# Performance work log

Measured on AMD Instinct MI355X. Metric: run time of the kernel, lower is better.

## Reference

```python
import jax, jax.numpy as jnp
import numpy as np

N_NODES = 50000
N_EDGES = 600000
DIN, DH, DOUT = 128, 256, 128
BN_EPS = 1e-5
LRELU_SLOPE = 0.01


def setup_inputs() -> dict:
    key = jax.random.key(0)
    ks = jax.random.split(key, 16)
    rn = lambda k, s, sc=0.05: jax.random.normal(k, s, dtype=jnp.float32) * sc
    return {
        'nodes': jax.random.normal(ks[0], (N_NODES, DIN), dtype=jnp.float32),
        'src': jax.random.randint(ks[1], (N_EDGES,), 0, N_NODES, dtype=jnp.int32),
        'dst': jax.random.randint(ks[2], (N_EDGES,), 0, N_NODES, dtype=jnp.int32),
        # FeedForward params
        'Wf1': rn(ks[3], (DIN, DH)), 'bf1': jnp.zeros((DH,), jnp.float32),
        'gf1': jnp.ones((DH,), jnp.float32), 'bef1': jnp.zeros((DH,), jnp.float32),
        'Wf2': rn(ks[4], (DH, DIN)), 'bf2': jnp.zeros((DIN,), jnp.float32),
        'gf2': jnp.ones((DIN,), jnp.float32), 'bef2': jnp.zeros((DIN,), jnp.float32),
        # SAGEConv 1 (in->hidden)
        'Ws1': rn(ks[5], (DIN, DH)), 'Wn1': rn(ks[6], (DIN, DH)), 'b1': jnp.zeros((DH,), jnp.float32),
        'gs1': jnp.ones((DH,), jnp.float32), 'bs1': jnp.zeros((DH,), jnp.float32),
        # SAGEConv 2 (hidden->out)
        'Ws2': rn(ks[7], (DH, DOUT)), 'Wn2': rn(ks[8], (DH, DOUT)), 'b2': jnp.zeros((DOUT,), jnp.float32),
        'gs2': jnp.ones((DOUT,), jnp.float32), 'bs2': jnp.zeros((DOUT,), jnp.float32),
    }


def _bn(x, gamma, beta):
    # BatchNorm1d, training mode: batch stats over node dim, biased variance
    mu = jnp.mean(x, axis=0)
    var = jnp.mean(jnp.square(x - mu), axis=0)
    return (x - mu) * jax.lax.rsqrt(var + BN_EPS) * gamma + beta


def _sage_mean(x, src, dst, Wself, Wneigh, bias):
    # DGL SAGEConv('mean'): out = x@Wself + mean_{src->dst}(x[src])@Wneigh + bias
    n = x.shape[0]
    deg = jax.ops.segment_sum(jnp.ones_like(src, dtype=x.dtype), dst, num_segments=n)
    agg = jax.ops.segment_sum(x[src], dst, num_segments=n)  # [N, d] irregular scatter-add
    h_neigh = agg / jnp.maximum(deg, 1.0)[:, None]
    return x @ Wself + h_neigh @ Wneigh + bias


def reference(nodes, src, dst, Wf1, bf1, gf1, bef1, Wf2, bf2, gf2, bef2,
              Ws1, Wn1, b1, gs1, bs1, Ws2, Wn2, b2, gs2, bs2):
    # FeedForward (dropout=0 -> identity)
    h = jax.nn.relu(_bn(nodes @ Wf1 + bf1, gf1, bef1))
    h = jax.nn.relu(_bn(h @ Wf2 + bf2, gf2, bef2))
    # SAGE layer 1
    h1 = _sage_mean(h, src, dst, Ws1, Wn1, b1)
    h1 = jax.nn.leaky_relu(_bn(h1, gs1, bs1), LRELU_SLOPE)
    # SAGE layer 2
    h2 = _sage_mean(h1, src, dst, Ws2, Wn2, b2)
    return jax.nn.leaky_relu(_bn(h2, gs2, bs2), LRELU_SLOPE)
```

## Files before the change

### kernel.cpp

```cpp
#include <hip/hip_runtime.h>

#define DIN 128
#define BN_EPS 1e-5f

typedef __attribute__((ext_vector_type(8))) short bf16x8;
typedef __attribute__((ext_vector_type(8))) unsigned short us8;
typedef __attribute__((ext_vector_type(4))) float f32x4;

__device__ __forceinline__ ushort f2bf(float f) {
    unsigned u = __float_as_uint(f);
    u += 0x7fffu + ((u >> 16) & 1u);
    return (ushort)(u >> 16);
}
__device__ __forceinline__ float bf2f(ushort h) {
    return __uint_as_float(((unsigned)h) << 16);
}

template<int KC, int NT, int STATS>
__global__ __launch_bounds__(256) void gemm_lds(
    const ushort* __restrict__ A, const ushort* __restrict__ BT,
    ushort* __restrict__ C, int mStrips, int N,
    float* __restrict__ gsums, float* __restrict__ gsqs)
{
    constexpr int K = KC * 32;
    constexpr int CPR = KC * 4;
    constexpr int LOGCPR = (KC == 4) ? 4 : 5;
    constexpr int LPL = KC / 4;
    __shared__ ushort abuf[16 * K];

    int tid = threadIdx.x;
    int lane = tid & 63;
    int w = tid >> 6;
    int cl = lane & 15, q = lane >> 4;
    int colBase = w * (16 * NT);
    int chBase = w * (16 * KC);

    bf16x8 bf[NT][KC];
    #pragma unroll
    for (int nt = 0; nt < NT; nt++) {
        const ushort* bp = BT + (long)(colBase + nt * 16 + cl) * K + q * 8;
        #pragma unroll
        for (int kc = 0; kc < KC; kc++)
            bf[nt][kc] = *(const bf16x8*)(bp + kc * 32);
    }

    float ssum[NT], ssq[NT];
    #pragma unroll
    for (int nt = 0; nt < NT; nt++) { ssum[nt] = 0.f; ssq[nt] = 0.f; }

    int totalSets = gridDim.x;
    int s0 = blockIdx.x;

    us8 stg[LPL];
    {
        const ushort* As = A + (long)s0 * 16 * K;
        #pragma unroll
        for (int u = 0; u < LPL; u++)
            stg[u] = *(const us8*)(As + (chBase + u * 64 + lane) * 8);
        #pragma unroll
        for (int u = 0; u < LPL; u++) {
            int ch = chBase + u * 64 + lane;
            int r = ch >> LOGCPR;
            int c = ch & (CPR - 1);
            *(us8*)(abuf + (((r << LOGCPR) + (c ^ (r & 7))) * 8)) = stg[u];
        }
    }
    __syncthreads();

    for (int s = s0; s < mStrips; s += totalSets) {
        int nxt = s + totalSets;
        bool more = nxt < mStrips;
        if (more) {
            const ushort* As = A + (long)nxt * 16 * K;
            #pragma unroll
            for (int u = 0; u < LPL; u++)
                stg[u] = *(const us8*)(As + (chBase + u * 64 + lane) * 8);
        }
        bf16x8 af[KC];
        #pragma unroll
        for (int kc = 0; kc < KC; kc++)
            af[kc] = *(const bf16x8*)(abuf + (((cl << LOGCPR) + ((kc * 4 + q) ^ (cl & 7))) * 8));
        f32x4 acc[NT] = {};
        #pragma unroll
        for (int kc = 0; kc < KC; kc++)
            #pragma unroll
            for (int nt = 0; nt < NT; nt++)
                acc[nt] = __builtin_amdgcn_mfma_f32_16x16x32_bf16(af[kc], bf[nt][kc], acc[nt], 0, 0, 0);
        int rowBase = s * 16;
        #pragma unroll
        for (int nt = 0; nt < NT; nt++) {
            #pragma unroll
            for (int r = 0; r < 4; r++) {
                float v = acc[nt][r];
                long row = rowBase + q * 4 + r;
                C[row * N + colBase + nt * 16 + cl] = f2bf(v);
                if (STATS) { ssum[nt] += v; ssq[nt] += v * v; }
            }
        }
        __syncthreads();
        if (more) {
            #pragma unroll
            for (int u = 0; u < LPL; u++) {
                int ch = chBase + u * 64 + lane;
                int r = ch >> LOGCPR;
                int c = ch & (CPR - 1);
                *(us8*)(abuf + (((r << LOGCPR) + (c ^ (r & 7))) * 8)) = stg[u];
            }
        }
        __syncthreads();
    }

    if (STATS) {
        #pragma unroll
        for (int nt = 0; nt < NT; nt++) {
            ssum[nt] += __shfl_xor(ssum[nt], 16, 64);
            ssum[nt] += __shfl_xor(ssum[nt], 32, 64);
            ssq[nt]  += __shfl_xor(ssq[nt], 16, 64);
            ssq[nt]  += __shfl_xor(ssq[nt], 32, 64);
        }
        if (q == 0) {
            #pragma unroll
            for (int nt = 0; nt < NT; nt++) {
                atomicAdd(&gsums[colBase + nt * 16 + cl], ssum[nt]);
                atomicAdd(&gsqs[colBase + nt * 16 + cl], ssq[nt]);
            }
        }
    }
}

__global__ __launch_bounds__(256) void setup_all(
    const float* __restrict__ nodes, ushort* __restrict__ Xbf, int nConv4, int nbConv,
    const float* __restrict__ W0, const float* __restrict__ W1,
    const float* __restrict__ W2, const float* __restrict__ W3,
    const float* __restrict__ W4, const float* __restrict__ W5,
    ushort* __restrict__ WT,
    int* __restrict__ zeroInts, int nZero4, int nbZero,
    float* __restrict__ stats)
{
    int b = blockIdx.x;
    int tid = threadIdx.x;
    if (b < nbConv) {
        int t = b * 256 + tid;
        if (t < nConv4) {
            float4 v = *(const float4*)&nodes[(long)t * 4];
            ushort4 o; o.x = f2bf(v.x); o.y = f2bf(v.y); o.z = f2bf(v.z); o.w = f2bf(v.w);
            *(ushort4*)&Xbf[(long)t * 4] = o;
        }
        return;
    }
    b -= nbConv;
    if (b < 768) {
        int seg = b >> 7;
        const float* W; int logK, dstBase, stride, kOff;
        switch (seg) {
            case 0: W = W0; logK = 7; dstBase = 0;      stride = 128; kOff = 0;   break;
            case 1: W = W1; logK = 8; dstBase = 32768;  stride = 256; kOff = 0;   break;
            case 2: W = W2; logK = 7; dstBase = 65536;  stride = 256; kOff = 0;   break;
            case 3: W = W3; logK = 7; dstBase = 65536;  stride = 256; kOff = 128; break;
            case 4: W = W4; logK = 8; dstBase = 131072; stride = 256; kOff = 0;   break;
            default:W = W5; logK = 8; dstBase = 163840; stride = 256; kOff = 0;   break;
        }
        int t = (b & 127) * 256 + tid;
        int N = 32768 >> logK;
        int k = t & ((1 << logK) - 1);
        int n = t >> logK;
        WT[(long)dstBase + (long)n * stride + kOff + k] = f2bf(W[(long)k * N + n]);
        return;
    }
    b -= 768;
    if (b < nbZero) {
        int t = b * 256 + tid;
        if (t < nZero4) *(int4*)&zeroInts[(long)t * 4] = make_int4(0, 0, 0, 0);
        return;
    }
    b -= nbZero;
    int t = b * 256 + tid;
    if (t < 512) *(float4*)&stats[(long)t * 4] = make_float4(0, 0, 0, 0);
}

template<int LOGN>
__global__ __launch_bounds__(256) void bnact_bf16(
    const ushort* __restrict__ X,
    const float* __restrict__ sums, const float* __restrict__ sqs,
    const float* __restrict__ gamma, const float* __restrict__ beta, float invM,
    ushort* __restrict__ O, int nRows, int outStride, float negSlope)
{
    constexpr int NCH = 1 << LOGN;
    __shared__ float ssc[NCH], ssh[NCH];
    int tid = threadIdx.x;
    if (tid < NCH) {
        float mean = sums[tid] * invM;
        float var = sqs[tid] * invM - mean * mean;
        float sc = gamma[tid] * rsqrtf(var + BN_EPS);
        ssc[tid] = sc;
        ssh[tid] = beta[tid] - mean * sc;
    }
    __syncthreads();
    int cb = (tid * 8) & (NCH - 1);
    float4 sA = *(const float4*)&ssc[cb];
    float4 sB = *(const float4*)&ssc[cb + 4];
    float4 hA = *(const float4*)&ssh[cb];
    float4 hB = *(const float4*)&ssh[cb + 4];
    const int rpb = (256 * 8) >> LOGN;
    int r0 = blockIdx.x * rpb + ((tid * 8) >> LOGN);
    int rstride = gridDim.x * rpb;
    for (int row = r0; row < nRows; row += rstride) {
        us8 v = *(const us8*)&X[(long)row * NCH + cb];
        float f0 = bf2f(v[0]) * sA.x + hA.x; f0 = (f0 > 0.f) ? f0 : f0 * negSlope;
        float f1 = bf2f(v[1]) * sA.y + hA.y; f1 = (f1 > 0.f) ? f1 : f1 * negSlope;
        float f2 = bf2f(v[2]) * sA.z + hA.z; f2 = (f2 > 0.f) ? f2 : f2 * negSlope;
        float f3 = bf2f(v[3]) * sA.w + hA.w; f3 = (f3 > 0.f) ? f3 : f3 * negSlope;
        float f4 = bf2f(v[4]) * sB.x + hB.x; f4 = (f4 > 0.f) ? f4 : f4 * negSlope;
        float f5 = bf2f(v[5]) * sB.y + hB.y; f5 = (f5 > 0.f) ? f5 : f5 * negSlope;
        float f6 = bf2f(v[6]) * sB.z + hB.z; f6 = (f6 > 0.f) ? f6 : f6 * negSlope;
        float f7 = bf2f(v[7]) * sB.w + hB.w; f7 = (f7 > 0.f) ? f7 : f7 * negSlope;
        us8 o;
        o[0] = f2bf(f0); o[1] = f2bf(f1); o[2] = f2bf(f2); o[3] = f2bf(f3);
        o[4] = f2bf(f4); o[5] = f2bf(f5); o[6] = f2bf(f6); o[7] = f2bf(f7);
        *(us8*)&O[(long)row * outStride + cb] = o;
    }
}

__global__ __launch_bounds__(256) void bnact_f32(
    float* __restrict__ X,
    const float* __restrict__ sums, const float* __restrict__ sqs,
    const float* __restrict__ gamma, const float* __restrict__ beta, float invM,
    int nRows, float negSlope)
{
    __shared__ float ssc[128], ssh[128];
    int tid = threadIdx.x;
    if (tid < 128) {
        float mean = sums[tid] * invM;
        float var = sqs[tid] * invM - mean * mean;
        float sc = gamma[tid] * rsqrtf(var + BN_EPS);
        ssc[tid] = sc;
        ssh[tid] = beta[tid] - mean * sc;
    }
    __syncthreads();
    int cb = (tid * 4) & 127;
    float4 sc = *(const float4*)&ssc[cb];
    float4 sh = *(const float4*)&ssh[cb];
    int r0 = blockIdx.x * 8 + ((tid * 4) >> 7);
    int rstride = gridDim.x * 8;
    for (int row = r0; row < nRows; row += rstride) {
        float4 v = *(const float4*)&X[(long)row * 128 + cb];
        float a = v.x * sc.x + sh.x; a = (a > 0.f) ? a : a * negSlope;
        float b = v.y * sc.y + sh.y; b = (b > 0.f) ? b : b * negSlope;
        float d = v.z * sc.z + sh.z; d = (d > 0.f) ? d : d * negSlope;
        float e = v.w * sc.w + sh.w; e = (e > 0.f) ? e : e * negSlope;
        *(float4*)&X[(long)row * 128 + cb] = make_float4(a, b, d, e);
    }
}

__global__ __launch_bounds__(256) void colstats128(
    const float* __restrict__ X, float* __restrict__ sums, float* __restrict__ sqs, int M)
{
    __shared__ float ss[128], sq[128];
    int tid = threadIdx.x;
    if (tid < 128) { ss[tid] = 0.f; sq[tid] = 0.f; }
    __syncthreads();
    int cg = tid & 31;
    int worker = (blockIdx.x << 3) | (tid >> 5);
    int totalW = gridDim.x << 3;
    float4 s4 = make_float4(0, 0, 0, 0), q4 = make_float4(0, 0, 0, 0);
    for (int r = worker; r < M; r += totalW) {
        float4 v = *(const float4*)&X[(long)r * 128 + cg * 4];
        s4.x += v.x; s4.y += v.y; s4.z += v.z; s4.w += v.w;
        q4.x += v.x * v.x; q4.y += v.y * v.y; q4.z += v.z * v.z; q4.w += v.w * v.w;
    }
    atomicAdd(&ss[cg * 4 + 0], s4.x); atomicAdd(&sq[cg * 4 + 0], q4.x);
    atomicAdd(&ss[cg * 4 + 1], s4.y); atomicAdd(&sq[cg * 4 + 1], q4.y);
    atomicAdd(&ss[cg * 4 + 2], s4.z); atomicAdd(&sq[cg * 4 + 2], q4.z);
    atomicAdd(&ss[cg * 4 + 3], s4.w); atomicAdd(&sq[cg * 4 + 3], q4.w);
    __syncthreads();
    if (tid < 128) { atomicAdd(&sums[tid], ss[tid]); atomicAdd(&sqs[tid], sq[tid]); }
}

__global__ void degcount_kernel(const int* __restrict__ dst, int* __restrict__ degi, int E)
{
    int i = blockIdx.x * blockDim.x + threadIdx.x;
    if (i < E) atomicAdd(&degi[dst[i]], 1);
}

__global__ __launch_bounds__(256) void scan_block_sums(const int* __restrict__ degi,
                                                       int* __restrict__ partial, int n)
{
    __shared__ int s[256];
    int i = blockIdx.x * 256 + threadIdx.x;
    s[threadIdx.x] = (i < n) ? degi[i] : 0;
    __syncthreads();
    for (int off = 128; off > 0; off >>= 1) {
        if (threadIdx.x < off) s[threadIdx.x] += s[threadIdx.x + off];
        __syncthreads();
    }
    if (threadIdx.x == 0) partial[blockIdx.x] = s[0];
}

__global__ __launch_bounds__(256) void scan_final(const int* __restrict__ degi,
                                                  const int* __restrict__ partial,
                                                  int* __restrict__ rowstart, int n, int nb)
{
    __shared__ int s[256];
    __shared__ int ps[256];
    int tid = threadIdx.x;
    ps[tid] = (tid < nb && tid < (int)blockIdx.x) ? partial[tid] : 0;
    __syncthreads();
    for (int off = 128; off > 0; off >>= 1) {
        if (tid < off) ps[tid] += ps[tid + off];
        __syncthreads();
    }
    int offset = ps[0];
    int i = blockIdx.x * 256 + tid;
    int v = (i < n) ? degi[i] : 0;
    s[tid] = v;
    __syncthreads();
    for (int off = 1; off < 256; off <<= 1) {
        int t = (tid >= off) ? s[tid - off] : 0;
        __syncthreads();
        s[tid] += t;
        __syncthreads();
    }
    if (i < n) rowstart[i] = offset + s[tid] - v;
}

__global__ void fillcsr_kernel(const int* __restrict__ src, const int* __restrict__ dst,
                               const int* __restrict__ rowstart, int* __restrict__ cursor,
                               int* __restrict__ csr, int E)
{
    int i = blockIdx.x * blockDim.x + threadIdx.x;
    if (i < E) {
        int d = dst[i];
        int p = atomicAdd(&cursor[d], 1);
        csr[rowstart[d] + p] = src[i];
    }
}

__device__ __forceinline__ void acc8(float acc[8], us8 v) {
    #pragma unroll
    for (int e = 0; e < 8; e++) acc[e] += bf2f(v[e]);
}

__global__ __launch_bounds__(256) void gather16_bf(
    const ushort* __restrict__ X, const int* __restrict__ rowstart,
    const int* __restrict__ degi, const int* __restrict__ csr,
    ushort* __restrict__ O, int nN)
{
    int wv = (blockIdx.x * blockDim.x + threadIdx.x) >> 6;
    int lane = threadIdx.x & 63;
    if (wv >= nN) return;
    int g = lane >> 4;
    int sc = lane & 15;
    int start = rowstart[wv], d = degi[wv];
    const ushort* Xc = X + sc * 8;
    float acc[8] = {};
    if (d > 0) {
        int dm = (d < 64) ? d : 64;
        int idx_l = csr[start + ((lane < dm) ? lane : (dm - 1))];
        int j = 0;
        for (; j + 8 <= dm; j += 8) {
            int i0 = __shfl(idx_l, j + g, 64);
            int i1 = __shfl(idx_l, j + 4 + g, 64);
            us8 v0 = *(const us8*)(Xc + (long)i0 * 256);
            us8 v1 = *(const us8*)(Xc + (long)i1 * 256);
            acc8(acc, v0);
            acc8(acc, v1);
        }
        if (j + 4 <= dm) {
            int i0 = __shfl(idx_l, j + g, 64);
            us8 v0 = *(const us8*)(Xc + (long)i0 * 256);
            acc8(acc, v0);
            j += 4;
        }
        int rem = dm - j;
        if (rem > 0) {
            int sl = j + ((g < rem) ? g : (rem - 1));
            int i0 = __shfl(idx_l, sl, 64);
            if (g < rem) {
                us8 v0 = *(const us8*)(Xc + (long)i0 * 256);
                acc8(acc, v0);
            }
        }
        for (int jj = 64; jj < d; jj += 4) {
            if (jj + g < d) {
                int i0 = csr[start + jj + g];
                us8 v0 = *(const us8*)(Xc + (long)i0 * 256);
                acc8(acc, v0);
            }
        }
    }
    #pragma unroll
    for (int e = 0; e < 8; e++) {
        acc[e] += __shfl_xor(acc[e], 16, 64);
        acc[e] += __shfl_xor(acc[e], 32, 64);
    }
    if (g == 0) {
        float inv = 1.f / fmaxf((float)d, 1.f);
        us8 o;
        #pragma unroll
        for (int e = 0; e < 8; e++) o[e] = f2bf(acc[e] * inv);
        *(us8*)(O + (long)wv * 256 + sc * 8) = o;
    }
}

__global__ __launch_bounds__(256) void gather16_fuse(
    const ushort* __restrict__ Z, const int* __restrict__ rowstart,
    const int* __restrict__ degi, const int* __restrict__ csr,
    float* __restrict__ O, int nN)
{
    int wv = (blockIdx.x * blockDim.x + threadIdx.x) >> 6;
    int lane = threadIdx.x & 63;
    if (wv >= nN) return;
    int g = lane >> 4;
    int sc = lane & 15;
    int start = rowstart[wv], d = degi[wv];
    const ushort* Zc = Z + sc * 8;
    us8 selfv = *(const us8*)(Zc + (long)wv * 256 + 128);
    float acc[8] = {};
    if (d > 0) {
        int dm = (d < 64) ? d : 64;
        int idx_l = csr[start + ((lane < dm) ? lane : (dm - 1))];
        int j = 0;
        for (; j + 8 <= dm; j += 8) {
            int i0 = __shfl(idx_l, j + g, 64);
            int i1 = __shfl(idx_l, j + 4 + g, 64);
            us8 v0 = *(const us8*)(Zc + (long)i0 * 256);
            us8 v1 = *(const us8*)(Zc + (long)i1 * 256);
            acc8(acc, v0);
            acc8(acc, v1);
        }
        if (j + 4 <= dm) {
            int i0 = __shfl(idx_l, j + g, 64);
            us8 v0 = *(const us8*)(Zc + (long)i0 * 256);
            acc8(acc, v0);
            j += 4;
        }
        int rem = dm - j;
        if (rem > 0) {
            int sl = j + ((g < rem) ? g : (rem - 1));
            int i0 = __shfl(idx_l, sl, 64);
            if (g < rem) {
                us8 v0 = *(const us8*)(Zc + (long)i0 * 256);
                acc8(acc, v0);
            }
        }
        for (int jj = 64; jj < d; jj += 4) {
            if (jj + g < d) {
                int i0 = csr[start + jj + g];
                us8 v0 = *(const us8*)(Zc + (long)i0 * 256);
                acc8(acc, v0);
            }
        }
    }
    #pragma unroll
    for (int e = 0; e < 8; e++) {
        acc[e] += __shfl_xor(acc[e], 16, 64);
        acc[e] += __shfl_xor(acc[e], 32, 64);
    }
    if (g == 0) {
        float inv = 1.f / fmaxf((float)d, 1.f);
        float r[8];
        #pragma unroll
        for (int e = 0; e < 8; e++) r[e] = acc[e] * inv + bf2f(selfv[e]);
        float* op = O + (long)wv * 128 + sc * 8;
        *(float4*)op = make_float4(r[0], r[1], r[2], r[3]);
        *(float4*)(op + 4) = make_float4(r[4], r[5], r[6], r[7]);
    }
}

extern "C" void kernel_launch(void* const* d_in, const int* in_sizes, int n_in,
                              void* d_out, int out_size, void* d_ws, size_t ws_size,
                              hipStream_t stream)
{
    const float* nodes = (const float*)d_in[0];
    const int*   src   = (const int*)d_in[1];
    const int*   dst   = (const int*)d_in[2];
    const float* Wf1   = (const float*)d_in[3];
    const float* gf1   = (const float*)d_in[5];
    const float* bef1  = (const float*)d_in[6];
    const float* Wf2   = (const float*)d_in[7];
    const float* gf2   = (const float*)d_in[9];
    const float* bef2  = (const float*)d_in[10];
    const float* Ws1   = (const float*)d_in[11];
    const float* Wn1   = (const float*)d_in[12];
    const float* gs1   = (const float*)d_in[14];
    const float* bs1   = (const float*)d_in[15];
    const float* Ws2   = (const float*)d_in[16];
    const float* Wn2   = (const float*)d_in[17];
    const float* gs2   = (const float*)d_in[19];
    const float* bs2   = (const float*)d_in[20];

    int nN = in_sizes[0] / DIN;
    int nE = in_sizes[1];
    float* out = (float*)d_out;
    int mStrips = nN / 16;
    float invM = 1.0f / nN;

    ushort* PRE = (ushort*)d_ws;
    ushort* BF1 = PRE + (size_t)nN * 256;
    ushort* BF2 = BF1 + (size_t)nN * 256;
    float* stats = (float*)(BF2 + (size_t)nN * 256);
    float* scale = stats + 2048;
    float* shift = scale + 256;
    ushort* WT   = (ushort*)(shift + 256);
    int* degi     = (int*)(WT + 196608);
    int* cursor   = degi + nN;
    int* rowstart = cursor + nN;
    int* partial  = rowstart + nN;
    int* csr      = partial + 256;

    ushort* Wf1T = WT;
    ushort* Wf2T = WT + 32768;
    ushort* Wc1T = WT + 65536;
    ushort* Wc2T = WT + 131072;

    dim3 blk(256);
    auto cdiv = [](int a, int b) { return (a + b - 1) / b; };
    int nScanBlocks = cdiv(nN, 256);

    int nConv4 = nN * DIN / 4;
    int nbConv = cdiv(nConv4, 256);
    int nZero4 = (2 * nN) / 4;
    int nbZero = cdiv(nZero4, 256);
    setup_all<<<dim3(nbConv + 768 + nbZero + 2), blk, 0, stream>>>(
        nodes, BF1, nConv4, nbConv,
        Wf1, Wf2, Ws1, Wn1, Wn2, Ws2, WT,
        degi, nZero4, nbZero, stats);

    degcount_kernel<<<dim3(cdiv(nE, 256)), blk, 0, stream>>>(dst, degi, nE);
    scan_block_sums<<<dim3(nScanBlocks), blk, 0, stream>>>(degi, partial, nN);
    scan_final<<<dim3(nScanBlocks), blk, 0, stream>>>(degi, partial, rowstart, nN, nScanBlocks);
    fillcsr_kernel<<<dim3(cdiv(nE, 256)), blk, 0, stream>>>(src, dst, rowstart, cursor, csr, nE);

    gemm_lds<4, 4, 1><<<dim3(512), blk, 0, stream>>>(BF1, Wf1T, PRE, mStrips, 256, stats, stats + 256);
    bnact_bf16<8><<<dim3(2048), blk, 0, stream>>>(PRE, stats, stats + 256, gf1, bef1, invM,
                                                  BF1, nN, 256, 0.0f);

    gemm_lds<8, 2, 1><<<dim3(512), blk, 0, stream>>>(BF1, Wf2T, PRE, mStrips, 128, stats + 512, stats + 768);
    bnact_bf16<7><<<dim3(2048), blk, 0, stream>>>(PRE, stats + 512, stats + 768, gf2, bef2, invM,
                                                  BF2, nN, 256, 0.0f);

    gather16_bf<<<dim3(cdiv(nN * 64, 256)), blk, 0, stream>>>(BF2, rowstart, degi, csr, BF2 + 128, nN);

    gemm_lds<8, 4, 1><<<dim3(512), blk, 0, stream>>>(BF2, Wc1T, PRE, mStrips, 256, stats + 1024, stats + 1280);
    bnact_bf16<8><<<dim3(2048), blk, 0, stream>>>(PRE, stats + 1024, stats + 1280, gs1, bs1, invM,
                                                  BF1, nN, 256, 0.01f);

    gemm_lds<8, 4, 0><<<dim3(512), blk, 0, stream>>>(BF1, Wc2T, BF2, mStrips, 256, nullptr, nullptr);
    gather16_fuse<<<dim3(cdiv(nN * 64, 256)), blk, 0, stream>>>(BF2, rowstart, degi, csr, out, nN);

    colstats128<<<dim3(120), blk, 0, stream>>>(out, stats + 1536, stats + 1792, nN);
    bnact_f32<<<dim3(2048), blk, 0, stream>>>(out, stats + 1536, stats + 1792, gs2, bs2, invM,
                                              nN, 0.01f);
}
```

Measured before the change: 372.3 us.

## Fuse BN+activation into next GEMM A-load with double-buffered LDS

Folds the batch-norm and activation that follow GEMM 1 and GEMM 3 into the A-tile staging of the next GEMM. Normalization happens on the fly as rows are written to LDS, which removes two standalone elementwise passes over the 256-wide activations. The GEMM also gains a double-buffered LDS tile with loads issued two strips ahead, and a column-group split (LOGNG) so the last GEMM runs with NT=2 over two block groups. Every block now recomputes the per-column BN scale and shift, and the extra work sits in the GEMM's load path, which may add register pressure.

```diff
diff --git a/kernel.cpp b/kernel.cpp
--- a/kernel.cpp
+++ b/kernel.cpp
@@ -16,23 +16,29 @@
     return __uint_as_float(((unsigned)h) << 16);
 }
 
-template<int KC, int NT, int STATS>
+template<int KC, int NT, int LOGNG, int STATS, int BNIN>
 __global__ __launch_bounds__(256) void gemm_lds(
     const ushort* __restrict__ A, const ushort* __restrict__ BT,
     ushort* __restrict__ C, int mStrips, int N,
-    float* __restrict__ gsums, float* __restrict__ gsqs)
+    float* __restrict__ gsums, float* __restrict__ gsqs,
+    const float* __restrict__ isums, const float* __restrict__ isqs,
+    const float* __restrict__ igam, const float* __restrict__ ibet,
+    float invM, float negSlope)
 {
     constexpr int K = KC * 32;
     constexpr int CPR = KC * 4;
     constexpr int LOGCPR = (KC == 4) ? 4 : 5;
     constexpr int LPL = KC / 4;
-    __shared__ ushort abuf[16 * K];
+    __shared__ ushort abuf[2][16 * K];
 
     int tid = threadIdx.x;
     int lane = tid & 63;
     int w = tid >> 6;
     int cl = lane & 15, q = lane >> 4;
-    int colBase = w * (16 * NT);
+    int grp = blockIdx.x & ((1 << LOGNG) - 1);
+    int s0 = blockIdx.x >> LOGNG;
+    int TT = gridDim.x >> LOGNG;
+    int colBase = grp * (4 * 16 * NT) + w * (16 * NT);
     int chBase = w * (16 * KC);
 
     bf16x8 bf[NT][KC];
@@ -44,71 +50,97 @@
             bf[nt][kc] = *(const bf16x8*)(bp + kc * 32);
     }
 
+    float sc8[8], sh8[8];
+    if (BNIN) {
+        int cb = ((chBase + lane) & (CPR - 1)) * 8;
+        #pragma unroll
+        for (int e = 0; e < 8; e++) {
+            float mean = isums[cb + e] * invM;
+            float var = isqs[cb + e] * invM - mean * mean;
+            float s = igam[cb + e] * rsqrtf(var + BN_EPS);
+            sc8[e] = s;
+            sh8[e] = ibet[cb + e] - mean * s;
+        }
+    }
+
     float ssum[NT], ssq[NT];
     #pragma unroll
     for (int nt = 0; nt < NT; nt++) { ssum[nt] = 0.f; ssq[nt] = 0.f; }
 
-    int totalSets = gridDim.x;
-    int s0 = blockIdx.x;
-
-    us8 stg[LPL];
-    {
-        const ushort* As = A + (long)s0 * 16 * K;
+    auto stage_load = [&](us8 (&stg)[LPL], int strip) {
+        const ushort* As = A + (long)strip * 16 * K;
         #pragma unroll
         for (int u = 0; u < LPL; u++)
             stg[u] = *(const us8*)(As + (chBase + u * 64 + lane) * 8);
+    };
+    auto stage_write = [&](int buf, us8 (&stg)[LPL]) {
         #pragma unroll
         for (int u = 0; u < LPL; u++) {
             int ch = chBase + u * 64 + lane;
             int r = ch >> LOGCPR;
             int c = ch & (CPR - 1);
-            *(us8*)(abuf + (((r << LOGCPR) + (c ^ (r & 7))) * 8)) = stg[u];
-        }
-    }
-    __syncthreads();
-
-    for (int s = s0; s < mStrips; s += totalSets) {
-        int nxt = s + totalSets;
-        bool more = nxt < mStrips;
-        if (more) {
-            const ushort* As = A + (long)nxt * 16 * K;
-            #pragma unroll
-            for (int u = 0; u < LPL; u++)
-                stg[u] = *(const us8*)(As + (chBase + u * 64 + lane) * 8);
-        }
-        bf16x8 af[KC];
-        #pragma unroll
-        for (int kc = 0; kc < KC; kc++)
-            af[kc] = *(const bf16x8*)(abuf + (((cl << LOGCPR) + ((kc * 4 + q) ^ (cl & 7))) * 8));
-        f32x4 acc[NT] = {};
-        #pragma unroll
-        for (int kc = 0; kc < KC; kc++)
-            #pragma unroll
-            for (int nt = 0; nt < NT; nt++)
-                acc[nt] = __builtin_amdgcn_mfma_f32_16x16x32_bf16(af[kc], bf[nt][kc], acc[nt], 0, 0, 0);
-        int rowBase = s * 16;
-        #pragma unroll
-        for (int nt = 0; nt < NT; nt++) {
-            #pragma unroll
-            for (int r = 0; r < 4; r++) {
-                float v = acc[nt][r];
-                long row = rowBase + q * 4 + r;
-                C[row * N + colBase + nt * 16 + cl] = f2bf(v);
-                if (STATS) { ssum[nt] += v; ssq[nt] += v * v; }
+            us8 v = stg[u];
+            if (BNIN) {
+                us8 o;
+                #pragma unroll
+                for (int e = 0; e < 8; e++) {
+                    float f = bf2f(v[e]) * sc8[e] + sh8[e];
+                    f = (f > 0.f) ? f : f * negSlope;
+                    o[e] = f2bf(f);
+                }
+                v = o;
             }
-        }
-        __syncthreads();
-        if (more) {
-            #pragma unroll
-            for (int u = 0; u < LPL; u++) {
-                int ch = chBase + u * 64 + lane;
-                int r = ch >> LOGCPR;
-                int c = ch & (CPR - 1);
-                *(us8*)(abuf + (((r << LOGCPR) + (c ^ (r & 7))) * 8)) = stg[u];
-            }
-        }
-        __syncthreads();
-    }
+            *(us8*)(abuf[buf] + (((r << LOGCPR) + (c ^ (r & 7))) * 8)) = v;
+        }
+    };
+
+    us8 stgA[LPL], stgB[LPL];
+    int s = s0;
+    stage_load(stgA, s);
+    if (s + TT < mStrips) stage_load(stgB, s + TT);
+    stage_write(0, stgA);
+    if (s + 2 * TT < mStrips) stage_load(stgA, s + 2 * TT);
+    __syncthreads();
+    int cur = 0;
+
+#define GEMM_STEP(STG)                                                                  \
+    {                                                                                   \
+        bf16x8 af[KC];                                                                  \
+        _Pragma("unroll")                                                               \
+        for (int kc = 0; kc < KC; kc++)                                                 \
+            af[kc] = *(const bf16x8*)(abuf[cur] +                                       \
+                     (((cl << LOGCPR) + ((kc * 4 + q) ^ (cl & 7))) * 8));               \
+        if (s + TT < mStrips) stage_write(cur ^ 1, STG);                                \
+        if (s + 3 * TT < mStrips) stage_load(STG, s + 3 * TT);                          \
+        f32x4 acc[NT] = {};                                                             \
+        _Pragma("unroll")                                                               \
+        for (int kc = 0; kc < KC; kc++)                                                 \
+            _Pragma("unroll")                                                           \
+            for (int nt = 0; nt < NT; nt++)                                             \
+                acc[nt] = __builtin_amdgcn_mfma_f32_16x16x32_bf16(af[kc], bf[nt][kc],   \
+                                                                  acc[nt], 0, 0, 0);    \
+        int rowBase = s * 16;                                                           \
+        _Pragma("unroll")                                                               \
+        for (int nt = 0; nt < NT; nt++) {                                               \
+            _Pragma("unroll")                                                           \
+            for (int r = 0; r < 4; r++) {                                               \
+                float v = acc[nt][r];                                                   \
+                long row = rowBase + q * 4 + r;                                         \
+                C[row * N + colBase + nt * 16 + cl] = f2bf(v);                          \
+                if (STATS) { ssum[nt] += v; ssq[nt] += v * v; }                         \
+            }                                                                           \
+        }                                                                               \
+        __syncthreads();                                                                \
+        s += TT; cur ^= 1;                                                              \
+    }
+
+    while (true) {
+        GEMM_STEP(stgB);
+        if (s >= mStrips) break;
+        GEMM_STEP(stgA);
+        if (s >= mStrips) break;
+    }
+#undef GEMM_STEP
 
     if (STATS) {
         #pragma unroll
@@ -531,21 +563,27 @@
     scan_final<<<dim3(nScanBlocks), blk, 0, stream>>>(degi, partial, rowstart, nN, nScanBlocks);
     fillcsr_kernel<<<dim3(cdiv(nE, 256)), blk, 0, stream>>>(src, dst, rowstart, cursor, csr, nE);
 
-    gemm_lds<4, 4, 1><<<dim3(512), blk, 0, stream>>>(BF1, Wf1T, PRE, mStrips, 256, stats, stats + 256);
-    bnact_bf16<8><<<dim3(2048), blk, 0, stream>>>(PRE, stats, stats + 256, gf1, bef1, invM,
-                                                  BF1, nN, 256, 0.0f);
-
-    gemm_lds<8, 2, 1><<<dim3(512), blk, 0, stream>>>(BF1, Wf2T, PRE, mStrips, 128, stats + 512, stats + 768);
-    bnact_bf16<7><<<dim3(2048), blk, 0, stream>>>(PRE, stats + 512, stats + 768, gf2, bef2, invM,
+    gemm_lds<4, 4, 0, 1, 0><<<dim3(512), blk, 0, stream>>>(
+        BF1, Wf1T, PRE, mStrips, 256, stats, stats + 256,
+        nullptr, nullptr, nullptr, nullptr, 0.f, 0.f);
+
+    gemm_lds<8, 2, 0, 1, 1><<<dim3(512), blk, 0, stream>>>(
+        PRE, Wf2T, BF1, mStrips, 128, stats + 512, stats + 768,
+        stats, stats + 256, gf1, bef1, invM, 0.0f);
+
+    bnact_bf16<7><<<dim3(2048), blk, 0, stream>>>(BF1, stats + 512, stats + 768, gf2, bef2, invM,
                                                   BF2, nN, 256, 0.0f);
 
     gather16_bf<<<dim3(cdiv(nN * 64, 256)), blk, 0, stream>>>(BF2, rowstart, degi, csr, BF2 + 128, nN);
 
-    gemm_lds<8, 4, 1><<<dim3(512), blk, 0, stream>>>(BF2, Wc1T, PRE, mStrips, 256, stats + 1024, stats + 1280);
-    bnact_bf16<8><<<dim3(2048), blk, 0, stream>>>(PRE, stats + 1024, stats + 1280, gs1, bs1, invM,
-                                                  BF1, nN, 256, 0.01f);
-
-    gemm_lds<8, 4, 0><<<dim3(512), blk, 0, stream>>>(BF1, Wc2T, BF2, mStrips, 256, nullptr, nullptr);
+    gemm_lds<8, 4, 0, 1, 0><<<dim3(512), blk, 0, stream>>>(
+        BF2, Wc1T, PRE, mStrips, 256, stats + 1024, stats + 1280,
+        nullptr, nullptr, nullptr, nullptr, 0.f, 0.f);
+
+    gemm_lds<8, 2, 1, 0, 1><<<dim3(512), blk, 0, stream>>>(
+        PRE, Wc2T, BF2, mStrips, 256, nullptr, nullptr,
+        stats + 1024, stats + 1280, gs1, bs1, invM, 0.01f);
+
     gather16_fuse<<<dim3(cdiv(nN * 64, 256)), blk, 0, stream>>>(BF2, rowstart, degi, csr, out, nN);
 
     colstats128<<<dim3(120), blk, 0, stream>>>(out, stats + 1536, stats + 1792, nN);
```

Result: faster. 355.5 us (-4.5%).
